# Kernel tuning notes

Measured on AMD Instinct MI355X. Metric: run time of the kernel, lower is better.

## Reference

```python
import jax, jax.numpy as jnp
import numpy as np


def next_fast_len(n: int) -> int:
    # smallest m >= n whose only prime factors are 2, 3, 5 (matches torch ref)
    if n <= 2:
        return 2
    def is_fast(m):
        for p in (2, 3, 5):
            while m % p == 0:
                m //= p
        return m == 1
    while not is_fast(n):
        n += 1
    return n


def setup_inputs() -> dict:
    key = jax.random.key(0)
    k1, k2 = jax.random.split(key)
    B, C, H, W = 4, 64, 251, 509
    u = jax.random.normal(k1, (B, C, H, W), dtype=jnp.float32)
    k = jax.random.normal(k2, (B, C, H, W), dtype=jnp.float32)
    return {"u": u, "k": k}


def reference(u, k):
    # FFT-based 2D long convolution (FlashFFTConvInterface fallback path):
    # zero-pad to 2/3/5-smooth sizes, orthonormal rfft2, pointwise complex
    # multiply, irfft2, crop back, cast to input dtype.
    B, C, H, W = u.shape
    Hp, Wp = next_fast_len(H), next_fast_len(W)
    pad = ((0, 0), (0, 0), (0, Hp - H), (0, Wp - W))
    u_f = jnp.fft.rfft2(jnp.pad(u, pad).astype(jnp.float32), norm="ortho")
    k_f = jnp.fft.rfft2(jnp.pad(k, pad).astype(jnp.float32), norm="ortho")
    y = jnp.fft.irfft2(u_f * k_f, s=(Hp, Wp), norm="ortho")
    return y[..., :H, :W].astype(u.dtype)
```

## Files before the change

kernel.cpp:

```cpp
#include <hip/hip_runtime.h>
#include <math.h>


#define H_IN 251
#define W_IN 509
#define NIMG 256
#define LROW 516
#define CSTR 264

__device__ __forceinline__ float2 cadd(float2 a, float2 b){ return make_float2(a.x+b.x, a.y+b.y); }
__device__ __forceinline__ float2 csub(float2 a, float2 b){ return make_float2(a.x-b.x, a.y-b.y); }
__device__ __forceinline__ float2 cmul(float2 a, float2 b){ return make_float2(a.x*b.x-a.y*b.y, a.x*b.y+a.y*b.x); }
__device__ __forceinline__ float2 mnegi(float2 a){ return make_float2(a.y, -a.x); }

__device__ __forceinline__ void dft8(float2 x[8]) {
    const float s = 0.70710678118654752f;
    float2 y0=cadd(x[0],x[4]), y4=csub(x[0],x[4]);
    float2 y1=cadd(x[1],x[5]), y5=csub(x[1],x[5]);
    float2 y2=cadd(x[2],x[6]), y6=csub(x[2],x[6]);
    float2 y3=cadd(x[3],x[7]), y7=csub(x[3],x[7]);
    y5 = cmul(y5, make_float2(s, -s));
    y6 = mnegi(y6);
    y7 = cmul(y7, make_float2(-s, -s));
    float2 z0=cadd(y0,y2), z2=csub(y0,y2);
    float2 z1=cadd(y1,y3), z3=mnegi(csub(y1,y3));
    float2 z4=cadd(y4,y6), z6=csub(y4,y6);
    float2 z5=cadd(y5,y7), z7=mnegi(csub(y5,y7));
    float2 p0=cadd(z0,z1), p1=csub(z0,z1);
    float2 p2=cadd(z2,z3), p3=csub(z2,z3);
    float2 p4=cadd(z4,z5), p5=csub(z4,z5);
    float2 p6=cadd(z6,z7), p7=csub(z6,z7);
    x[0]=p0; x[1]=p4; x[2]=p2; x[3]=p6; x[4]=p1; x[5]=p5; x[6]=p3; x[7]=p7;
}

__device__ __forceinline__ void dft4(float2 x[4]) {
    float2 a=cadd(x[0],x[2]), c=csub(x[0],x[2]);
    float2 b=cadd(x[1],x[3]), d=mnegi(csub(x[1],x[3]));
    float2 p0=cadd(a,b), p1=csub(a,b);
    float2 p2=cadd(c,d), p3=csub(c,d);
    x[0]=p0; x[1]=p2; x[2]=p1; x[3]=p3;
}

__device__ __forceinline__ void tw8(float2 v[8], float ang1) {
    #pragma unroll
    for (int q = 1; q < 8; ++q) {
        float sn, cs; __sincosf(ang1 * (float)q, &sn, &cs);
        v[q] = cmul(v[q], make_float2(cs, sn));
    }
}

__global__ __launch_bounds__(512, 4) void kA(const float* __restrict__ u,
                                             const float* __restrict__ kk,
                                             float2* __restrict__ zt,
                                             int img_base) {
    __shared__ float2 lds[8][LROW];
    const int imgl = blockIdx.x >> 5;
    const int h0   = (blockIdx.x & 31) << 3;
    const int rr   = threadIdx.x >> 6;
    const int t    = threadIdx.x & 63;
    const int h    = h0 + rr;
    const int img  = img_base + imgl;

    float2 X[8];
    {
        const size_t rowoff = ((size_t)img * H_IN + h) * W_IN;
        #pragma unroll
        for (int r = 0; r < 8; ++r) {
            const int w = t + (r << 6);
            float2 v = make_float2(0.f, 0.f);
            if (h < H_IN && w < W_IN) v = make_float2(u[rowoff + w], kk[rowoff + w]);
            X[r] = v;
        }
    }
    dft8(X);
    tw8(X, -6.2831853071795864f * (float)t / 512.0f);
    #pragma unroll
    for (int q = 0; q < 8; ++q) lds[rr][(q << 6) + (t ^ (q << 3))] = X[q];
    __syncthreads();

    const int q  = t >> 3;
    const int j1 = t & 7;
    float2 Y[8];
    #pragma unroll
    for (int j2 = 0; j2 < 8; ++j2)
        Y[j2] = lds[rr][(q << 6) + ((j1 + (j2 << 3)) ^ (q << 3))];
    dft8(Y);
    tw8(Y, -6.2831853071795864f * (float)j1 / 64.0f);
    __syncthreads();
    #pragma unroll
    for (int q2 = 0; q2 < 8; ++q2) lds[rr][(j1 << 6) + (q2 << 3) + q] = Y[q2];
    __syncthreads();

    const int q2 = t & 7;
    float2 Z[8];
    #pragma unroll
    for (int j = 0; j < 8; ++j) Z[j] = lds[rr][(j << 6) + (q2 << 3) + q];
    dft8(Z);
    __syncthreads();
    #pragma unroll
    for (int q3 = 0; q3 < 8; ++q3) lds[rr][(q3 << 6) + (q2 << 3) + q] = Z[q3];
    __syncthreads();

    for (int idx = threadIdx.x; idx < 8 * 512; idx += 512) {
        const int w  = idx >> 3;
        const int hh = idx & 7;
        zt[((size_t)imgl * 512 + w) * 256 + (size_t)(h0 + hh)] = lds[hh][w];
    }
}

__global__ __launch_bounds__(256, 4) void kB(float2* __restrict__ zt) {
    __shared__ float2 spec[8][CSTR];
    const int imgl = blockIdx.x / 65;
    const int bq   = blockIdx.x - imgl * 65;
    const int c    = threadIdx.x >> 5;
    const int t    = threadIdx.x & 31;
    const int pi   = c >> 1, side = c & 1;
    const int g    = (bq << 2) + pi;
    const bool valid = (g <= 256);
    const bool selfp = (g == 0) || (g == 256);
    const int w    = side ? ((512 - g) & 511) : g;
    const size_t colbase = ((size_t)imgl * 512 + w) * 256;

    float2 X[8];
    #pragma unroll
    for (int r = 0; r < 8; ++r) X[r] = zt[colbase + t + (r << 5)];

    const int q  = t >> 2;
    const int j1 = t & 3;
    const int rrq = t & 3;

    dft8(X);
    tw8(X, -6.2831853071795864f * (float)t / 256.0f);
    #pragma unroll
    for (int qq = 0; qq < 8; ++qq) spec[c][(qq << 5) + (t ^ ((qq & 3) << 3))] = X[qq];
    __syncthreads();

    float2 Y[8];
    #pragma unroll
    for (int j2 = 0; j2 < 8; ++j2)
        Y[j2] = spec[c][(q << 5) + ((j1 + (j2 << 2)) ^ ((q & 3) << 3))];
    dft8(Y);
    tw8(Y, -6.2831853071795864f * (float)j1 / 32.0f);
    __syncthreads();
    #pragma unroll
    for (int q2 = 0; q2 < 8; ++q2) spec[c][(j1 << 6) + (q2 << 3) + q] = Y[q2];
    __syncthreads();

    float2 Za[4], Zb[4];
    #pragma unroll
    for (int j = 0; j < 4; ++j) Za[j] = spec[c][(j << 6) + (rrq << 3) + q];
    #pragma unroll
    for (int j = 0; j < 4; ++j) Zb[j] = spec[c][(j << 6) + ((rrq + 4) << 3) + q];
    dft4(Za); dft4(Zb);
    __syncthreads();
    #pragma unroll
    for (int k = 0; k < 4; ++k) spec[c][(k << 6) + (rrq << 3) + q] = Za[k];
    #pragma unroll
    for (int k = 0; k < 4; ++k) spec[c][(k << 6) + ((rrq + 4) << 3) + q] = Zb[k];
    __syncthreads();

    {
        const int ti = threadIdx.x & 63;
        const int cA = (threadIdx.x >> 6) << 1;
        #pragma unroll
        for (int hi = 0; hi < 4; ++hi) {
            const int h  = ti + (hi << 6);
            const int hm = (256 - h) & 255;
            const float2 Zf = spec[cA][h];
            const float2 Zm = spec[cA + 1][hm];
            const float2 U = make_float2(0.5f * (Zf.x + Zm.x),  0.5f * (Zf.y - Zm.y));
            const float2 K = make_float2(0.5f * (Zf.y + Zm.y), -0.5f * (Zf.x - Zm.x));
            const float2 P = cmul(U, K);
            spec[cA][h]      = P;
            spec[cA + 1][hm] = make_float2(P.x, -P.y);
        }
    }
    __syncthreads();

    #pragma unroll
    for (int r = 0; r < 8; ++r) {
        float2 v = spec[c][t + (r << 5)];
        X[r] = make_float2(v.x, -v.y);
    }
    __syncthreads();
    dft8(X);
    tw8(X, -6.2831853071795864f * (float)t / 256.0f);
    #pragma unroll
    for (int qq = 0; qq < 8; ++qq) spec[c][(qq << 5) + (t ^ ((qq & 3) << 3))] = X[qq];
    __syncthreads();
    #pragma unroll
    for (int j2 = 0; j2 < 8; ++j2)
        Y[j2] = spec[c][(q << 5) + ((j1 + (j2 << 2)) ^ ((q & 3) << 3))];
    dft8(Y);
    tw8(Y, -6.2831853071795864f * (float)j1 / 32.0f);
    __syncthreads();
    #pragma unroll
    for (int q2 = 0; q2 < 8; ++q2) spec[c][(j1 << 6) + (q2 << 3) + q] = Y[q2];
    __syncthreads();
    #pragma unroll
    for (int j = 0; j < 4; ++j) Za[j] = spec[c][(j << 6) + (rrq << 3) + q];
    #pragma unroll
    for (int j = 0; j < 4; ++j) Zb[j] = spec[c][(j << 6) + ((rrq + 4) << 3) + q];
    dft4(Za); dft4(Zb);
    __syncthreads();
    #pragma unroll
    for (int k = 0; k < 4; ++k)
        spec[c][(k << 6) + (rrq << 3) + q] = make_float2(Za[k].x, -Za[k].y);
    #pragma unroll
    for (int k = 0; k < 4; ++k)
        spec[c][(k << 6) + ((rrq + 4) << 3) + q] = make_float2(Zb[k].x, -Zb[k].y);
    __syncthreads();

    if (valid && !(side && selfp)) {
        #pragma unroll
        for (int r = 0; r < 8; ++r) {
            const int h = t + (r << 5);
            zt[colbase + h] = spec[c][h];
        }
    }
}

__global__ __launch_bounds__(512, 4) void kC(const float2* __restrict__ zt,
                                             float* __restrict__ y,
                                             int img_base) {
    __shared__ float2 lds[8][LROW];
    const int imgl = blockIdx.x >> 5;
    const int h0   = (blockIdx.x & 31) << 3;
    const int rr   = threadIdx.x >> 6;
    const int t    = threadIdx.x & 63;
    const int img  = img_base + imgl;

    for (int idx = threadIdx.x; idx < 8 * 512; idx += 512) {
        const int w  = idx >> 3;
        const int hh = idx & 7;
        lds[hh][w] = zt[((size_t)imgl * 512 + w) * 256 + (size_t)(h0 + hh)];
    }
    __syncthreads();

    float2 X[8];
    #pragma unroll
    for (int r = 0; r < 8; ++r) {
        float2 v = lds[rr][t + (r << 6)];
        X[r] = make_float2(v.x, -v.y);
    }
    __syncthreads();

    dft8(X);
    tw8(X, -6.2831853071795864f * (float)t / 512.0f);
    #pragma unroll
    for (int q = 0; q < 8; ++q) lds[rr][(q << 6) + (t ^ (q << 3))] = X[q];
    __syncthreads();

    const int q  = t >> 3;
    const int j1 = t & 7;
    float2 Y[8];
    #pragma unroll
    for (int j2 = 0; j2 < 8; ++j2)
        Y[j2] = lds[rr][(q << 6) + ((j1 + (j2 << 3)) ^ (q << 3))];
    dft8(Y);
    tw8(Y, -6.2831853071795864f * (float)j1 / 64.0f);
    __syncthreads();
    #pragma unroll
    for (int q2 = 0; q2 < 8; ++q2) lds[rr][(j1 << 6) + (q2 << 3) + q] = Y[q2];
    __syncthreads();

    const int q2 = t & 7;
    float2 Z[8];
    #pragma unroll
    for (int j = 0; j < 8; ++j) Z[j] = lds[rr][(j << 6) + (q2 << 3) + q];
    dft8(Z);
    __syncthreads();
    #pragma unroll
    for (int q3 = 0; q3 < 8; ++q3) lds[rr][(q3 << 6) + (q2 << 3) + q] = Z[q3];
    __syncthreads();

    const float scale = 2.1073424255447017e-08f;
    for (int idx = threadIdx.x; idx < 8 * 512; idx += 512) {
        const int w  = idx & 511;
        const int hh = idx >> 9;
        const int h  = h0 + hh;
        if (h < H_IN && w < W_IN)
            y[((size_t)img * H_IN + h) * W_IN + w] = lds[hh][w].x * scale;
    }
}

extern "C" void kernel_launch(void* const* d_in, const int* in_sizes, int n_in,
                              void* d_out, int out_size, void* d_ws, size_t ws_size,
                              hipStream_t stream) {
    const float* u = (const float*)d_in[0];
    const float* k = (const float*)d_in[1];
    float* y = (float*)d_out;
    float2* zt = (float2*)d_ws;

    const size_t per_img = (size_t)512 * 256 * sizeof(float2);
    int chunk = (int)(ws_size / per_img);
    if (chunk > NIMG) chunk = NIMG;
    if (chunk < 1) chunk = 1;

    for (int base = 0; base < NIMG; base += chunk) {
        const int nimg = (NIMG - base < chunk) ? (NIMG - base) : chunk;
        kA<<<dim3(nimg * 32), dim3(512), 0, stream>>>(u, k, zt, base);
        kB<<<dim3(nimg * 65), dim3(256), 0, stream>>>(zt);
        kC<<<dim3(nimg * 32), dim3(512), 0, stream>>>(zt, y, base);
    }
}
```

Measured before the change: 563.8 us.

## Use wave barriers, recurrence twiddles, LDS swizzle, float4 transposes, XCD block swizzle

Replaces block-wide __syncthreads with wave-level barriers wherever each wavefront only touches its own LDS row or column. It also computes the twiddles for each radix-8 stage from a single sincos by complex multiplication, and XOR-swizzles LDS indices to reduce bank conflicts. The global transpose stores and loads move to float4 pairs of rows, blocks are remapped so neighbouring work shares an XCD, and kB's occupancy hint is raised. The risks are wave-barrier correctness, which depends on each row being owned by one wave, and small twiddle accuracy drift from the recurrence.

```diff
diff --git a/kernel.cpp b/kernel.cpp
--- a/kernel.cpp
+++ b/kernel.cpp
@@ -7,6 +7,8 @@
 #define NIMG 256
 #define LROW 516
 #define CSTR 264
+
+#define WBAR() __builtin_amdgcn_wave_barrier()
 
 __device__ __forceinline__ float2 cadd(float2 a, float2 b){ return make_float2(a.x+b.x, a.y+b.y); }
 __device__ __forceinline__ float2 csub(float2 a, float2 b){ return make_float2(a.x-b.x, a.y-b.y); }
@@ -42,11 +44,21 @@
 }
 
 __device__ __forceinline__ void tw8(float2 v[8], float ang1) {
-    #pragma unroll
-    for (int q = 1; q < 8; ++q) {
-        float sn, cs; __sincosf(ang1 * (float)q, &sn, &cs);
-        v[q] = cmul(v[q], make_float2(cs, sn));
-    }
+    float sn, cs; __sincosf(ang1, &sn, &cs);
+    const float2 w1 = make_float2(cs, sn);
+    const float2 w2 = cmul(w1, w1);
+    const float2 w3 = cmul(w2, w1);
+    const float2 w4 = cmul(w2, w2);
+    const float2 w5 = cmul(w4, w1);
+    const float2 w6 = cmul(w4, w2);
+    const float2 w7 = cmul(w4, w3);
+    v[1] = cmul(v[1], w1); v[2] = cmul(v[2], w2); v[3] = cmul(v[3], w3);
+    v[4] = cmul(v[4], w4); v[5] = cmul(v[5], w5); v[6] = cmul(v[6], w6);
+    v[7] = cmul(v[7], w7);
+}
+
+__device__ __forceinline__ int xcd_pair_swizzle(int b) {
+    return (b & ~15) | ((b & 7) << 1) | ((b >> 3) & 1);
 }
 
 __global__ __launch_bounds__(512, 4) void kA(const float* __restrict__ u,
@@ -54,8 +66,9 @@
                                              float2* __restrict__ zt,
                                              int img_base) {
     __shared__ float2 lds[8][LROW];
-    const int imgl = blockIdx.x >> 5;
-    const int h0   = (blockIdx.x & 31) << 3;
+    const int wk   = xcd_pair_swizzle(blockIdx.x);
+    const int imgl = wk >> 5;
+    const int h0   = (wk & 31) << 3;
     const int rr   = threadIdx.x >> 6;
     const int t    = threadIdx.x & 63;
     const int h    = h0 + rr;
@@ -76,7 +89,7 @@
     tw8(X, -6.2831853071795864f * (float)t / 512.0f);
     #pragma unroll
     for (int q = 0; q < 8; ++q) lds[rr][(q << 6) + (t ^ (q << 3))] = X[q];
-    __syncthreads();
+    WBAR();
 
     const int q  = t >> 3;
     const int j1 = t & 7;
@@ -86,29 +99,36 @@
         Y[j2] = lds[rr][(q << 6) + ((j1 + (j2 << 3)) ^ (q << 3))];
     dft8(Y);
     tw8(Y, -6.2831853071795864f * (float)j1 / 64.0f);
-    __syncthreads();
-    #pragma unroll
-    for (int q2 = 0; q2 < 8; ++q2) lds[rr][(j1 << 6) + (q2 << 3) + q] = Y[q2];
-    __syncthreads();
+    WBAR();
+    #pragma unroll
+    for (int q2 = 0; q2 < 8; ++q2)
+        lds[rr][((j1 << 6) + (q2 << 3) + q) ^ ((j1 & 1) << 3)] = Y[q2];
+    WBAR();
 
     const int q2 = t & 7;
     float2 Z[8];
     #pragma unroll
-    for (int j = 0; j < 8; ++j) Z[j] = lds[rr][(j << 6) + (q2 << 3) + q];
+    for (int j = 0; j < 8; ++j)
+        Z[j] = lds[rr][((j << 6) + (q2 << 3) + q) ^ ((j & 1) << 3)];
     dft8(Z);
+    WBAR();
+    #pragma unroll
+    for (int q3 = 0; q3 < 8; ++q3)
+        lds[rr][((q3 << 6) + (q2 << 3) + q) ^ ((q3 & 1) << 3)] = Z[q3];
     __syncthreads();
-    #pragma unroll
-    for (int q3 = 0; q3 < 8; ++q3) lds[rr][(q3 << 6) + (q2 << 3) + q] = Z[q3];
-    __syncthreads();
-
-    for (int idx = threadIdx.x; idx < 8 * 512; idx += 512) {
-        const int w  = idx >> 3;
-        const int hh = idx & 7;
-        zt[((size_t)imgl * 512 + w) * 256 + (size_t)(h0 + hh)] = lds[hh][w];
-    }
-}
-
-__global__ __launch_bounds__(256, 4) void kB(float2* __restrict__ zt) {
+
+    for (int idx = threadIdx.x; idx < 8 * 256; idx += 512) {
+        const int w   = idx >> 2;
+        const int hh2 = (idx & 3) << 1;
+        const int wz  = w ^ (((w >> 6) & 1) << 3);
+        const float2 a = lds[hh2][wz];
+        const float2 b = lds[hh2 + 1][wz];
+        reinterpret_cast<float4*>(zt)[((size_t)imgl * 512 + w) * 128 + ((h0 + hh2) >> 1)] =
+            make_float4(a.x, a.y, b.x, b.y);
+    }
+}
+
+__global__ __launch_bounds__(256, 6) void kB(float2* __restrict__ zt) {
     __shared__ float2 spec[8][CSTR];
     const int imgl = blockIdx.x / 65;
     const int bq   = blockIdx.x - imgl * 65;
@@ -133,7 +153,7 @@
     tw8(X, -6.2831853071795864f * (float)t / 256.0f);
     #pragma unroll
     for (int qq = 0; qq < 8; ++qq) spec[c][(qq << 5) + (t ^ ((qq & 3) << 3))] = X[qq];
-    __syncthreads();
+    WBAR();
 
     float2 Y[8];
     #pragma unroll
@@ -141,10 +161,10 @@
         Y[j2] = spec[c][(q << 5) + ((j1 + (j2 << 2)) ^ ((q & 3) << 3))];
     dft8(Y);
     tw8(Y, -6.2831853071795864f * (float)j1 / 32.0f);
-    __syncthreads();
+    WBAR();
     #pragma unroll
     for (int q2 = 0; q2 < 8; ++q2) spec[c][(j1 << 6) + (q2 << 3) + q] = Y[q2];
-    __syncthreads();
+    WBAR();
 
     float2 Za[4], Zb[4];
     #pragma unroll
@@ -152,12 +172,12 @@
     #pragma unroll
     for (int j = 0; j < 4; ++j) Zb[j] = spec[c][(j << 6) + ((rrq + 4) << 3) + q];
     dft4(Za); dft4(Zb);
-    __syncthreads();
+    WBAR();
     #pragma unroll
     for (int k = 0; k < 4; ++k) spec[c][(k << 6) + (rrq << 3) + q] = Za[k];
     #pragma unroll
     for (int k = 0; k < 4; ++k) spec[c][(k << 6) + ((rrq + 4) << 3) + q] = Zb[k];
-    __syncthreads();
+    WBAR();
 
     {
         const int ti = threadIdx.x & 63;
@@ -175,41 +195,41 @@
             spec[cA + 1][hm] = make_float2(P.x, -P.y);
         }
     }
-    __syncthreads();
+    WBAR();
 
     #pragma unroll
     for (int r = 0; r < 8; ++r) {
         float2 v = spec[c][t + (r << 5)];
         X[r] = make_float2(v.x, -v.y);
     }
-    __syncthreads();
+    WBAR();
     dft8(X);
     tw8(X, -6.2831853071795864f * (float)t / 256.0f);
     #pragma unroll
     for (int qq = 0; qq < 8; ++qq) spec[c][(qq << 5) + (t ^ ((qq & 3) << 3))] = X[qq];
-    __syncthreads();
+    WBAR();
     #pragma unroll
     for (int j2 = 0; j2 < 8; ++j2)
         Y[j2] = spec[c][(q << 5) + ((j1 + (j2 << 2)) ^ ((q & 3) << 3))];
     dft8(Y);
     tw8(Y, -6.2831853071795864f * (float)j1 / 32.0f);
-    __syncthreads();
+    WBAR();
     #pragma unroll
     for (int q2 = 0; q2 < 8; ++q2) spec[c][(j1 << 6) + (q2 << 3) + q] = Y[q2];
-    __syncthreads();
+    WBAR();
     #pragma unroll
     for (int j = 0; j < 4; ++j) Za[j] = spec[c][(j << 6) + (rrq << 3) + q];
     #pragma unroll
     for (int j = 0; j < 4; ++j) Zb[j] = spec[c][(j << 6) + ((rrq + 4) << 3) + q];
     dft4(Za); dft4(Zb);
-    __syncthreads();
+    WBAR();
     #pragma unroll
     for (int k = 0; k < 4; ++k)
         spec[c][(k << 6) + (rrq << 3) + q] = make_float2(Za[k].x, -Za[k].y);
     #pragma unroll
     for (int k = 0; k < 4; ++k)
         spec[c][(k << 6) + ((rrq + 4) << 3) + q] = make_float2(Zb[k].x, -Zb[k].y);
-    __syncthreads();
+    WBAR();
 
     if (valid && !(side && selfp)) {
         #pragma unroll
@@ -224,16 +244,20 @@
                                              float* __restrict__ y,
                                              int img_base) {
     __shared__ float2 lds[8][LROW];
-    const int imgl = blockIdx.x >> 5;
-    const int h0   = (blockIdx.x & 31) << 3;
+    const int wk   = xcd_pair_swizzle(blockIdx.x);
+    const int imgl = wk >> 5;
+    const int h0   = (wk & 31) << 3;
     const int rr   = threadIdx.x >> 6;
     const int t    = threadIdx.x & 63;
     const int img  = img_base + imgl;
 
-    for (int idx = threadIdx.x; idx < 8 * 512; idx += 512) {
-        const int w  = idx >> 3;
-        const int hh = idx & 7;
-        lds[hh][w] = zt[((size_t)imgl * 512 + w) * 256 + (size_t)(h0 + hh)];
+    for (int idx = threadIdx.x; idx < 8 * 256; idx += 512) {
+        const int w   = idx >> 2;
+        const int hh2 = (idx & 3) << 1;
+        const float4 v = reinterpret_cast<const float4*>(zt)
+            [((size_t)imgl * 512 + w) * 128 + ((h0 + hh2) >> 1)];
+        lds[hh2][w]     = make_float2(v.x, v.y);
+        lds[hh2 + 1][w] = make_float2(v.z, v.w);
     }
     __syncthreads();
 
@@ -243,13 +267,13 @@
         float2 v = lds[rr][t + (r << 6)];
         X[r] = make_float2(v.x, -v.y);
     }
-    __syncthreads();
+    WBAR();
 
     dft8(X);
     tw8(X, -6.2831853071795864f * (float)t / 512.0f);
     #pragma unroll
     for (int q = 0; q < 8; ++q) lds[rr][(q << 6) + (t ^ (q << 3))] = X[q];
-    __syncthreads();
+    WBAR();
 
     const int q  = t >> 3;
     const int j1 = t & 7;
@@ -259,19 +283,22 @@
         Y[j2] = lds[rr][(q << 6) + ((j1 + (j2 << 3)) ^ (q << 3))];
     dft8(Y);
     tw8(Y, -6.2831853071795864f * (float)j1 / 64.0f);
-    __syncthreads();
-    #pragma unroll
-    for (int q2 = 0; q2 < 8; ++q2) lds[rr][(j1 << 6) + (q2 << 3) + q] = Y[q2];
-    __syncthreads();
+    WBAR();
+    #pragma unroll
+    for (int q2 = 0; q2 < 8; ++q2)
+        lds[rr][((j1 << 6) + (q2 << 3) + q) ^ ((j1 & 1) << 3)] = Y[q2];
+    WBAR();
 
     const int q2 = t & 7;
     float2 Z[8];
     #pragma unroll
-    for (int j = 0; j < 8; ++j) Z[j] = lds[rr][(j << 6) + (q2 << 3) + q];
+    for (int j = 0; j < 8; ++j)
+        Z[j] = lds[rr][((j << 6) + (q2 << 3) + q) ^ ((j & 1) << 3)];
     dft8(Z);
-    __syncthreads();
-    #pragma unroll
-    for (int q3 = 0; q3 < 8; ++q3) lds[rr][(q3 << 6) + (q2 << 3) + q] = Z[q3];
+    WBAR();
+    #pragma unroll
+    for (int q3 = 0; q3 < 8; ++q3)
+        lds[rr][((q3 << 6) + (q2 << 3) + q) ^ ((q3 & 1) << 3)] = Z[q3];
     __syncthreads();
 
     const float scale = 2.1073424255447017e-08f;
@@ -280,7 +307,8 @@
         const int hh = idx >> 9;
         const int h  = h0 + hh;
         if (h < H_IN && w < W_IN)
-            y[((size_t)img * H_IN + h) * W_IN + w] = lds[hh][w].x * scale;
+            y[((size_t)img * H_IN + h) * W_IN + w] =
+                lds[hh][w ^ (((w >> 6) & 1) << 3)].x * scale;
     }
 }
 
```

After: 554.1 us. About the same (-1.7%).
